# Kernel optimization log

Measured on AMD Instinct MI355X. Metric: run time of the kernel, lower is better.

Reference implementation:

```python
import jax, jax.numpy as jnp
import numpy as np

N, E = 20000, 640000
S_DIM, V_DIM, E_DIM = 128, 32 // 2, 32
EPS = 1e-8


def _vector_norm(v):
    # v: [N, V, 3] -> [N, V]
    return jnp.sqrt(jnp.clip((v * v).sum(-1), EPS))


def _gvp(s, v, W1, b1, W2, b2, Wv, Wg, bg):
    """SimpleGVP: s [N,s_in], v [N,v_in,3] -> (s_out [N,s_out], v_out [N,v_out,3]).
    Weights stored [in, out] (transpose of torch Linear)."""
    vn = _vector_norm(v)                                   # [N, v_in]
    h = jnp.concatenate([s, vn], axis=-1) @ W1 + b1        # [N, s_out]
    s_out = jax.nn.silu(h) @ W2 + b2                       # [N, s_out]
    v_proj = jnp.einsum('nvc,vw->nwc', v, Wv)              # [N, v_out, 3]
    gate = jax.nn.sigmoid(s_out @ Wg + bg)[..., None]      # [N, v_out, 1]
    return s_out, v_proj * gate


def _layer_norm(x, g, b, eps=1e-5):
    mu = x.mean(-1, keepdims=True)
    var = ((x - mu) ** 2).mean(-1, keepdims=True)
    return (x - mu) * jax.lax.rsqrt(var + eps) * g + b


def _linear_params(key, fan_in, fan_out, bias=True):
    kw, kb = jax.random.split(key)
    lim = 1.0 / np.sqrt(fan_in)
    W = jax.random.uniform(kw, (fan_in, fan_out), jnp.float32, -lim, lim)
    if bias:
        b = jax.random.uniform(kb, (fan_out,), jnp.float32, -lim, lim)
        return W, b
    return (W,)


def setup_inputs() -> dict:
    key = jax.random.key(0)
    ks = jax.random.split(key, 16)
    s = jax.random.normal(ks[0], (N, S_DIM), jnp.float32)
    v = jax.random.normal(ks[1], (N, V_DIM, 3), jnp.float32)
    edge_index = jax.random.randint(ks[2], (2, E), 0, N, jnp.int32)
    edge_s = jax.random.normal(ks[3], (E, E_DIM), jnp.float32)
    edge_v = jax.random.normal(ks[4], (E, 1, 3), jnp.float32)

    # message GVP: s_in = 2*S + E_DIM + 1 (+v_in norms), v_in = 2*V + 1
    ms_in, mv_in = 2 * S_DIM + E_DIM + 1, 2 * V_DIM + 1
    msg_W1, msg_b1 = _linear_params(ks[5], ms_in + mv_in, S_DIM)
    msg_W2, msg_b2 = _linear_params(ks[6], S_DIM, S_DIM)
    (msg_Wv,) = _linear_params(ks[7], mv_in, V_DIM, bias=False)
    msg_Wg, msg_bg = _linear_params(ks[8], S_DIM, V_DIM)

    # update GVP: s_in = 2*S, v_in = 2*V
    us_in, uv_in = 2 * S_DIM, 2 * V_DIM
    upd_W1, upd_b1 = _linear_params(ks[9], us_in + uv_in, S_DIM)
    upd_W2, upd_b2 = _linear_params(ks[10], S_DIM, S_DIM)
    (upd_Wv,) = _linear_params(ks[11], uv_in, V_DIM, bias=False)
    upd_Wg, upd_bg = _linear_params(ks[12], S_DIM, V_DIM)

    ln_g = jnp.ones((S_DIM,), jnp.float32)
    ln_b = jnp.zeros((S_DIM,), jnp.float32)

    return dict(s=s, v=v, edge_index=edge_index, edge_s=edge_s, edge_v=edge_v,
                msg_W1=msg_W1, msg_b1=msg_b1, msg_W2=msg_W2, msg_b2=msg_b2,
                msg_Wv=msg_Wv, msg_Wg=msg_Wg, msg_bg=msg_bg,
                upd_W1=upd_W1, upd_b1=upd_b1, upd_W2=upd_W2, upd_b2=upd_b2,
                upd_Wv=upd_Wv, upd_Wg=upd_Wg, upd_bg=upd_bg,
                ln_g=ln_g, ln_b=ln_b)


def reference(s, v, edge_index, edge_s, edge_v,
              msg_W1, msg_b1, msg_W2, msg_b2, msg_Wv, msg_Wg, msg_bg,
              upd_W1, upd_b1, upd_W2, upd_b2, upd_Wv, upd_Wg, upd_bg,
              ln_g, ln_b):
    src, dst = edge_index[0], edge_index[1]
    n = s.shape[0]

    # 1) per-edge message inputs (gather)
    edge_len = _vector_norm(edge_v)                                   # [E, 1]
    m_s_in = jnp.concatenate([s[src], s[dst], edge_s, edge_len], -1)  # [E, 2S+e+1]
    m_v_in = jnp.concatenate([v[src], v[dst], edge_v], 1)             # [E, 2V+1, 3]
    m_s, m_v = _gvp(m_s_in, m_v_in, msg_W1, msg_b1, msg_W2, msg_b2,
                    msg_Wv, msg_Wg, msg_bg)

    # 2) scatter-add aggregation at destination nodes
    agg_s = jax.ops.segment_sum(m_s, dst, num_segments=n)             # [N, S]
    agg_v = jax.ops.segment_sum(m_v, dst, num_segments=n)             # [N, V, 3]

    # 3) residual update
    u_s_in = jnp.concatenate([s, agg_s], -1)
    u_v_in = jnp.concatenate([v, agg_v], 1)
    ds, dv = _gvp(u_s_in, u_v_in, upd_W1, upd_b1, upd_W2, upd_b2,
                  upd_Wv, upd_Wg, upd_bg)

    s_out = _layer_norm(s + ds, ln_g, ln_b)
    v_out = v + dv
    return s_out, v_out
```

## Files before the change

kernel.cpp:

```cpp
#include <hip/hip_runtime.h>

typedef __attribute__((ext_vector_type(4))) float floatx4;
typedef __attribute__((ext_vector_type(8))) short shortx8;
typedef __attribute__((ext_vector_type(4))) short shortx4;
typedef __attribute__((ext_vector_type(4))) int intx4;
typedef __attribute__((ext_vector_type(2))) int intx2;

#define DEVI static __device__ __forceinline__

constexpr int NN = 20000;
constexpr int NE = 640000;

constexpr size_t W1ET_OFF = 0;
constexpr size_t WLEN_OFF = 8192;
constexpr size_t WCAT_OFF = 8704;
constexpr size_t W2GT_OFF = 90624;
constexpr size_t CG_OFF   = 94720;
constexpr size_t U1T_OFF  = 94784;
constexpr size_t B2U_OFF  = 168512;
constexpr size_t U2T_OFF  = 169024;
constexpr size_t UGT_OFF  = 201792;
constexpr size_t ASRC_OFF = 205888;
constexpr size_t ADST_OFF = ASRC_OFF + (size_t)NN * 128 * 2;
constexpr size_t BSRC_OFF = ADST_OFF + (size_t)NN * 128 * 2;
constexpr size_t BDST_OFF = BSRC_OFF + (size_t)NN * 64 * 2;
constexpr size_t AGG_S_OFF = BDST_OFF + (size_t)NN * 64 * 2;
constexpr size_t AGG_V_OFF = AGG_S_OFF + (size_t)NN * 128 * 2;
constexpr size_t CNT_OFF  = AGG_V_OFF + (size_t)NN * 64 * 2;
constexpr size_t OFF_OFF  = CNT_OFF + (size_t)NN * 4;
constexpr size_t PERM_OFF = OFF_OFF + (size_t)NN * 4;
constexpr size_t MEMSET_BYTES = (size_t)NN * 128 * 2 + (size_t)NN * 64 * 2 + (size_t)NN * 4;

DEVI float bf2f(short h) {
  union { unsigned u; float f; } c;
  c.u = ((unsigned)(unsigned short)h) << 16;
  return c.f;
}
DEVI short f2bf(float f) {
  union { float f; unsigned u; } c; c.f = f;
  unsigned x = c.u;
  return (short)((x + 0x7fffu + ((x >> 16) & 1u)) >> 16);
}
DEVI int pack2bf(float x, float y) {
  return (int)(unsigned short)f2bf(x) | ((int)(unsigned short)f2bf(y) << 16);
}
DEVI void atom_pk(short* addr, int val) {
  asm volatile("global_atomic_pk_add_bf16 %0, %1, off" : : "v"(addr), "v"(val) : "memory");
}
DEVI float sigm(float x) { return __builtin_amdgcn_rcpf(1.0f + __expf(-x)); }

DEVI floatx4 mfma16(shortx8 a, shortx8 b, floatx4 c) {
  return __builtin_amdgcn_mfma_f32_16x16x32_bf16(a, b, c, 0, 0, 0);
}

__global__ void gvp_prep(const float* __restrict__ mW1, const float* __restrict__ mW2,
                         const float* __restrict__ mWg, const float* __restrict__ mb2,
                         const float* __restrict__ mbg, const float* __restrict__ uW1,
                         const float* __restrict__ uW2, const float* __restrict__ uWg,
                         short* __restrict__ w1et, float* __restrict__ wlen,
                         short* __restrict__ wcat, short* __restrict__ w2gt,
                         float* __restrict__ cg, short* __restrict__ u1t,
                         float* __restrict__ b2u, short* __restrict__ u2t,
                         short* __restrict__ ugt) {
  int i = blockIdx.x * 256 + threadIdx.x;
  if (i < 4096) { int n = i >> 5, k = i & 31; w1et[i] = f2bf(mW1[(256 + k) * 128 + n]); return; }
  i -= 4096;
  if (i < 128) { wlen[i] = mW1[288 * 128 + i] + mW1[321 * 128 + i]; return; }
  i -= 128;
  if (i < 40960) {
    int n = i / 160, k = i % 160;
    float val = 0.f;
    if (n < 128) {
      if (k < 128) val = mW1[k * 128 + n];
      else if (k < 144) val = mW1[(161 + k) * 128 + n];
    } else {
      int n2 = n - 128;
      if (k < 128) val = mW1[(128 + k) * 128 + n2];
      else if (k < 144) val = mW1[(177 + k) * 128 + n2];
    }
    wcat[i] = f2bf(val);
    return;
  }
  i -= 40960;
  if (i < 2048) {
    int g = i >> 7, k = i & 127;
    float acc = 0.f;
#pragma unroll 4
    for (int c4 = 0; c4 < 32; ++c4) {
      floatx4 wr = *(const floatx4*)(mW2 + k * 128 + c4 * 4);
      acc += wr[0] * mWg[(c4 * 4 + 0) * 16 + g] + wr[1] * mWg[(c4 * 4 + 1) * 16 + g] +
             wr[2] * mWg[(c4 * 4 + 2) * 16 + g] + wr[3] * mWg[(c4 * 4 + 3) * 16 + g];
    }
    w2gt[i] = f2bf(acc);
    return;
  }
  i -= 2048;
  if (i < 16) {
    float acc = mbg[i];
    for (int c = 0; c < 128; ++c) acc += mb2[c] * mWg[c * 16 + i];
    cg[i] = acc;
    return;
  }
  i -= 16;
  if (i < 36864) {
    int n = i / 288, k = i % 288;
    if (k < 128 || k >= 256) {
      u1t[i] = f2bf(uW1[k * 128 + n]);
    } else {
      int j = k - 128;
      float acc = 0.f;
#pragma unroll 4
      for (int c4 = 0; c4 < 32; ++c4) {
        floatx4 wr = *(const floatx4*)(mW2 + j * 128 + c4 * 4);
        acc += wr[0] * uW1[(128 + c4 * 4 + 0) * 128 + n] +
               wr[1] * uW1[(128 + c4 * 4 + 1) * 128 + n] +
               wr[2] * uW1[(128 + c4 * 4 + 2) * 128 + n] +
               wr[3] * uW1[(128 + c4 * 4 + 3) * 128 + n];
      }
      u1t[i] = f2bf(acc);
    }
    return;
  }
  i -= 36864;
  if (i < 128) {
    float acc = 0.f;
    for (int c = 0; c < 128; ++c) acc += mb2[c] * uW1[(128 + c) * 128 + i];
    b2u[i] = acc;
    return;
  }
  i -= 128;
  if (i < 16384) { int n = i >> 7, k = i & 127; u2t[i] = f2bf(uW2[k * 128 + n]); return; }
  i -= 16384;
  if (i < 2048) { int g = i >> 7, k = i & 127; ugt[i] = f2bf(uWg[k * 16 + g]); return; }
}

__global__ void gvp_hist(const int* __restrict__ eidx, int* __restrict__ cnt) {
  int e = blockIdx.x * 256 + threadIdx.x;
  if (e < NE) atomicAdd(cnt + eidx[NE + e], 1);
}

__global__ void gvp_scan(const int* __restrict__ cnt, int* __restrict__ off) {
  __shared__ int part[256];
  const int t = threadIdx.x;
  const int base = t * 79;
  int sum = 0;
  for (int j = 0; j < 79; ++j) {
    int i = base + j;
    if (i < NN) sum += cnt[i];
  }
  part[t] = sum;
  __syncthreads();
  if (t == 0) {
    int run = 0;
    for (int i = 0; i < 256; ++i) { int c = part[i]; part[i] = run; run += c; }
  }
  __syncthreads();
  int run = part[t];
  for (int j = 0; j < 79; ++j) {
    int i = base + j;
    if (i < NN) { off[i] = run; run += cnt[i]; }
  }
}

__global__ void gvp_scatter(const int* __restrict__ eidx, int* __restrict__ off,
                            int* __restrict__ perm) {
  int e = blockIdx.x * 256 + threadIdx.x;
  if (e >= NE) return;
  int d = eidx[NE + e];
  int pos = atomicAdd(off + d, 1);
  perm[pos] = e;
}

__global__ __launch_bounds__(256) void gvp_nodepre(
    const float* __restrict__ s, const float* __restrict__ v,
    const short* __restrict__ wcat, const float* __restrict__ b1,
    const float* __restrict__ wv, short* __restrict__ Asrc,
    short* __restrict__ Adst, short* __restrict__ Bsrc, short* __restrict__ Bdst) {
  __shared__ __align__(16) short lx[64 * 160];
  const int tid = threadIdx.x;
  const int wid = tid >> 6;
  const int lane = tid & 63;
  const int quad = lane >> 4;
  const int l16 = lane & 15;
  const int nb0 = blockIdx.x * 64;

  intx4 z4 = {0, 0, 0, 0};
#pragma unroll
  for (int i = 0; i < 4; i++) {
    int idx = tid + i * 256;
    int r = idx >> 4, cc = (idx & 15) * 8;
    int node = nb0 + r;
    union { short sh[8]; intx4 v4; } u;
    u.v4 = z4;
    if (node < NN) {
      const float* sp = s + (size_t)node * 128 + cc;
      floatx4 f0 = *(const floatx4*)sp, f1 = *(const floatx4*)(sp + 4);
#pragma unroll
      for (int j = 0; j < 4; j++) { u.sh[j] = f2bf(f0[j]); u.sh[4 + j] = f2bf(f1[j]); }
    }
    *(intx4*)(lx + r * 160 + cc) = u.v4;
  }
  if (tid < 64) {
    int node = nb0 + tid;
    union { short sh[16]; intx4 v4[2]; } u;
#pragma unroll
    for (int j = 0; j < 16; j++) {
      float nv = 0.f;
      if (node < NN) {
        const float* vp = v + (size_t)node * 48 + j * 3;
        nv = sqrtf(fmaxf(vp[0] * vp[0] + vp[1] * vp[1] + vp[2] * vp[2], 1e-8f));
      }
      u.sh[j] = f2bf(nv);
    }
    *(intx4*)(lx + tid * 160 + 128) = u.v4[0];
    *(intx4*)(lx + tid * 160 + 136) = u.v4[1];
    *(intx4*)(lx + tid * 160 + 144) = z4;
    *(intx4*)(lx + tid * 160 + 152) = z4;
  }
  __syncthreads();

  floatx4 acc[16] = {};
#pragma unroll
  for (int kc = 0; kc < 5; kc++) {
    shortx8 a = *(const shortx8*)(lx + (wid * 16 + l16) * 160 + kc * 32 + quad * 8);
#pragma unroll
    for (int nt = 0; nt < 16; nt++) {
      shortx8 b = *(const shortx8*)(wcat + (size_t)(nt * 16 + l16) * 160 + kc * 32 + quad * 8);
      acc[nt] = mfma16(a, b, acc[nt]);
    }
  }

  float b1v[8];
#pragma unroll
  for (int nt = 0; nt < 8; nt++) b1v[nt] = b1[nt * 16 + l16];
#pragma unroll
  for (int i = 0; i < 4; i++) {
    int row = wid * 16 + quad * 4 + i;
    int node = nb0 + row;
    if (node < NN) {
      union { short sh[8]; intx4 v4; } us, ud;
#pragma unroll
      for (int nt = 0; nt < 8; nt++) {
        us.sh[nt] = f2bf(acc[nt][i] + b1v[nt]);
        ud.sh[nt] = f2bf(acc[8 + nt][i]);
      }
      *(intx4*)(Asrc + (size_t)node * 128 + l16 * 8) = us.v4;
      *(intx4*)(Adst + (size_t)node * 128 + l16 * 8) = ud.v4;
    }
  }

  {
    int node = nb0 + (tid >> 2), sub = tid & 3;
    if (node < NN) {
      float vr[48];
      const float* vp = v + (size_t)node * 48;
#pragma unroll
      for (int j = 0; j < 48; j++) vr[j] = vp[j];
      for (int w = sub * 4; w < sub * 4 + 4; w++) {
        float bs0 = 0, bs1 = 0, bs2 = 0, bd0 = 0, bd1 = 0, bd2 = 0;
#pragma unroll
        for (int j = 0; j < 16; j++) {
          float w0 = wv[j * 16 + w], w1 = wv[(16 + j) * 16 + w];
          bs0 += vr[j * 3 + 0] * w0; bs1 += vr[j * 3 + 1] * w0; bs2 += vr[j * 3 + 2] * w0;
          bd0 += vr[j * 3 + 0] * w1; bd1 += vr[j * 3 + 1] * w1; bd2 += vr[j * 3 + 2] * w1;
        }
        union { short sh[4]; intx2 v2; } ub, ud2;
        ub.sh[0] = f2bf(bs0); ub.sh[1] = f2bf(bs1); ub.sh[2] = f2bf(bs2); ub.sh[3] = 0;
        ud2.sh[0] = f2bf(bd0); ud2.sh[1] = f2bf(bd1); ud2.sh[2] = f2bf(bd2); ud2.sh[3] = 0;
        *(intx2*)(Bsrc + (size_t)node * 64 + w * 4) = ub.v2;
        *(intx2*)(Bdst + (size_t)node * 64 + w * 4) = ud2.v2;
      }
    }
  }
}

__global__ __launch_bounds__(256, 8) void gvp_edge(
    const int* __restrict__ perm, const int* __restrict__ eidx,
    const float* __restrict__ ev, const float* __restrict__ es,
    const short* __restrict__ w1et, const float* __restrict__ wlen,
    const short* __restrict__ w2gt, const short* __restrict__ Asrc,
    const short* __restrict__ Adst, const short* __restrict__ Bsrc,
    const short* __restrict__ Bdst, const float* __restrict__ cg,
    const float* __restrict__ wv, short* __restrict__ agg_s,
    short* __restrict__ agg_v) {
  __shared__ __align__(16) short lh_all[4 * 16 * 136];
  __shared__ int lpe[64];
  __shared__ int lsrc[64];
  __shared__ int ldst[64];
  __shared__ float lev4[64][4];

  const int tid = threadIdx.x;
  const int wid = tid >> 6;
  const int lane = tid & 63;
  const int quad = lane >> 4;
  const int l16 = lane & 15;
  const int e0 = blockIdx.x * 64;

  if (tid < 64) {
    int pe = perm[e0 + tid];
    lpe[tid] = pe;
    lsrc[tid] = eidx[pe];
    ldst[tid] = eidx[NE + pe];
  } else if (tid < 128) {
    int er = tid - 64;
    int pe = perm[e0 + er];
    const float* evp = ev + (size_t)pe * 3;
    float x = evp[0], y = evp[1], z = evp[2];
    lev4[er][0] = x; lev4[er][1] = y; lev4[er][2] = z;
    lev4[er][3] = sqrtf(fmaxf(x * x + y * y + z * z, 1e-8f));
  }
  __syncthreads();

  short* lh = lh_all + wid * 2176;

  const int erow = wid * 16 + l16;
  const int pe = lpe[erow];
  const float* ep = es + (size_t)pe * 32 + quad * 8;
  floatx4 ea = *(const floatx4*)ep;
  floatx4 eb = *(const floatx4*)(ep + 4);
  shortx8 afrag;
#pragma unroll
  for (int j = 0; j < 4; j++) { afrag[j] = f2bf(ea[j]); afrag[4 + j] = f2bf(eb[j]); }
  floatx4 acc[8];
#pragma unroll
  for (int nt = 0; nt < 8; nt++) {
    shortx8 b = *(const shortx8*)(w1et + (nt * 16 + l16) * 32 + quad * 8);
    floatx4 z = {0.f, 0.f, 0.f, 0.f};
    acc[nt] = mfma16(afrag, b, z);
  }

  int srcn[4], dstn[4];
  float lenr[4];
#pragma unroll
  for (int i = 0; i < 4; i++) {
    int r = wid * 16 + quad * 4 + i;
    srcn[i] = lsrc[r]; dstn[i] = ldst[r]; lenr[i] = lev4[r][3];
  }

#pragma unroll
  for (int i = 0; i < 4; i++) {
    shortx8 s8 = *(const shortx8*)(Asrc + (size_t)srcn[i] * 128 + l16 * 8);
    shortx8 d8 = *(const shortx8*)(Adst + (size_t)dstn[i] * 128 + l16 * 8);
#pragma unroll
    for (int nt = 0; nt < 8; nt++) acc[nt][i] += bf2f(s8[nt]) + bf2f(d8[nt]);
  }
#pragma unroll
  for (int nt = 0; nt < 8; nt++) {
    float wl = wlen[nt * 16 + l16];
#pragma unroll
    for (int i = 0; i < 4; i++) acc[nt][i] += lenr[i] * wl;
  }

#pragma unroll
  for (int nt = 0; nt < 8; nt++)
#pragma unroll
    for (int i = 0; i < 4; i++) {
      float h = acc[nt][i];
      lh[(quad * 4 + i) * 136 + nt * 16 + l16] = f2bf(h * sigm(h));
    }

  floatx4 acc3 = {0.f, 0.f, 0.f, 0.f};
#pragma unroll
  for (int kc = 0; kc < 4; kc++) {
    shortx8 a = *(const shortx8*)(lh + l16 * 136 + kc * 32 + quad * 8);
    shortx8 b = *(const shortx8*)(w2gt + l16 * 128 + kc * 32 + quad * 8);
    acc3 = mfma16(a, b, acc3);
  }

  float wv32v = wv[32 * 16 + l16];
  float cgv = cg[l16];
  float gv[4][3];
#pragma unroll
  for (int i = 0; i < 4; i++) {
    int r = wid * 16 + quad * 4 + i;
    shortx4 bs = *(const shortx4*)(Bsrc + (size_t)srcn[i] * 64 + l16 * 4);
    shortx4 bd = *(const shortx4*)(Bdst + (size_t)dstn[i] * 64 + l16 * 4);
    float vx = bf2f(bs[0]) + bf2f(bd[0]) + lev4[r][0] * wv32v;
    float vy = bf2f(bs[1]) + bf2f(bd[1]) + lev4[r][1] * wv32v;
    float vz = bf2f(bs[2]) + bf2f(bd[2]) + lev4[r][2] * wv32v;
    float g = sigm(acc3[i] + cgv);
    gv[i][0] = g * vx; gv[i][1] = g * vy; gv[i][2] = g * vz;
  }

  const int rbase = wid * 16;
  int r = 0;
  while (r < 16) {
    int d = ldst[rbase + r];
    int r2 = r + 1;
    while (r2 < 16 && ldst[rbase + r2] == d) ++r2;
    float s0 = 0.f, s1 = 0.f;
    for (int row = r; row < r2; ++row) {
      int pv = *(const int*)(lh + row * 136 + 2 * lane);
      s0 += bf2f((short)(pv & 0xffff));
      s1 += bf2f((short)((unsigned)pv >> 16));
    }
    atom_pk(agg_s + (size_t)d * 128 + 2 * lane, pack2bf(s0, s1));
    float vx = 0.f, vy = 0.f, vz = 0.f;
#pragma unroll
    for (int i = 0; i < 4; ++i) {
      int row = quad * 4 + i;
      if (row >= r && row < r2) { vx += gv[i][0]; vy += gv[i][1]; vz += gv[i][2]; }
    }
    vx += __shfl_xor(vx, 16); vy += __shfl_xor(vy, 16); vz += __shfl_xor(vz, 16);
    vx += __shfl_xor(vx, 32); vy += __shfl_xor(vy, 32); vz += __shfl_xor(vz, 32);
    if (quad == 0) {
      short* ap = agg_v + (size_t)d * 64 + l16 * 4;
      atom_pk(ap, pack2bf(vx, vy));
      atom_pk(ap + 2, pack2bf(vz, 0.f));
    }
    r = r2;
  }
}

__global__ __launch_bounds__(256) void gvp_node(
    const float* __restrict__ s, const float* __restrict__ v,
    const short* __restrict__ agg_s, const short* __restrict__ agg_v,
    const int* __restrict__ cnt, const float* __restrict__ b2u,
    const short* __restrict__ u1t, const short* __restrict__ u2t,
    const short* __restrict__ ugt, const float* __restrict__ b1,
    const float* __restrict__ b2, const float* __restrict__ uwv,
    const float* __restrict__ bg, const float* __restrict__ lng,
    const float* __restrict__ lnb, float* __restrict__ out_s,
    float* __restrict__ out_v) {
  __shared__ __align__(16) short lx[64 * 352];
  const int tid = threadIdx.x;
  const int wid = tid >> 6;
  const int lane = tid & 63;
  const int quad = lane >> 4;
  const int l16 = lane & 15;
  const int nb0 = blockIdx.x * 64;

  float cntf[4];
#pragma unroll
  for (int i = 0; i < 4; i++) {
    int node = nb0 + wid * 16 + quad * 4 + i;
    cntf[i] = (node < NN) ? (float)cnt[node] : 0.f;
  }

  intx4 z4 = {0, 0, 0, 0};
#pragma unroll
  for (int i = 0; i < 4; i++) {
    int idx = tid + i * 256;
    int r = idx >> 4, cc = (idx & 15) * 8;
    int node = nb0 + r;
    union { short sh[8]; intx4 v4; } u;
    u.v4 = z4;
    if (node < NN) {
      const float* sp = s + (size_t)node * 128 + cc;
      floatx4 f0 = *(const floatx4*)sp, f1 = *(const floatx4*)(sp + 4);
#pragma unroll
      for (int j = 0; j < 4; j++) { u.sh[j] = f2bf(f0[j]); u.sh[4 + j] = f2bf(f1[j]); }
    }
    *(intx4*)(lx + r * 288 + cc) = u.v4;
  }
#pragma unroll
  for (int i = 0; i < 4; i++) {
    int idx = tid + i * 256;
    int r = idx >> 4, cc = (idx & 15) * 8;
    int node = nb0 + r;
    intx4 val = z4;
    if (node < NN) val = *(const intx4*)(agg_s + (size_t)node * 128 + cc);
    *(intx4*)(lx + r * 288 + 128 + cc) = val;
  }
  {
    int r = tid >> 2, p = tid & 3;
    int node = nb0 + r;
    int w0 = (p & 1) * 8;
    if (p < 2) {
#pragma unroll
      for (int w = 0; w < 8; w++) {
        float nv = 0.f;
        if (node < NN) {
          const float* vp = v + (size_t)node * 48 + (w0 + w) * 3;
          nv = sqrtf(fmaxf(vp[0] * vp[0] + vp[1] * vp[1] + vp[2] * vp[2], 1e-8f));
        }
        lx[r * 288 + 256 + w0 + w] = f2bf(nv);
      }
    } else {
#pragma unroll
      for (int w = 0; w < 8; w++) {
        float nv = 0.f;
        if (node < NN) {
          const short* ap = agg_v + (size_t)node * 64 + (w0 + w) * 4;
          float x = bf2f(ap[0]), y = bf2f(ap[1]), zz = bf2f(ap[2]);
          nv = sqrtf(fmaxf(x * x + y * y + zz * zz, 1e-8f));
        }
        lx[r * 288 + 272 + w0 + w] = f2bf(nv);
      }
    }
  }
  __syncthreads();

  floatx4 acc[8] = {};
#pragma unroll
  for (int kc = 0; kc < 9; kc++) {
    shortx8 a = *(const shortx8*)(lx + (wid * 16 + l16) * 288 + kc * 32 + quad * 8);
#pragma unroll
    for (int nt = 0; nt < 8; nt++) {
      shortx8 b = *(const shortx8*)(u1t + (size_t)(nt * 16 + l16) * 288 + kc * 32 + quad * 8);
      acc[nt] = mfma16(a, b, acc[nt]);
    }
  }
  __syncthreads();

  short* lh = lx;
#pragma unroll
  for (int nt = 0; nt < 8; nt++)
#pragma unroll
    for (int i = 0; i < 4; i++) {
      int row = wid * 16 + quad * 4 + i;
      int col = nt * 16 + l16;
      float h = acc[nt][i] + b1[col] + cntf[i] * b2u[col];
      lh[row * 136 + col] = f2bf(h * sigm(h));
    }

  floatx4 acc2[8] = {};
#pragma unroll
  for (int kc = 0; kc < 4; kc++) {
    shortx8 a = *(const shortx8*)(lh + (wid * 16 + l16) * 136 + kc * 32 + quad * 8);
#pragma unroll
    for (int nt = 0; nt < 8; nt++) {
      shortx8 b = *(const shortx8*)(u2t + (size_t)(nt * 16 + l16) * 128 + kc * 32 + quad * 8);
      acc2[nt] = mfma16(a, b, acc2[nt]);
    }
  }

#pragma unroll
  for (int nt = 0; nt < 8; nt++)
#pragma unroll
    for (int i = 0; i < 4; i++) {
      int row = wid * 16 + quad * 4 + i;
      int col = nt * 16 + l16;
      int node = nb0 + row;
      float ds = acc2[nt][i] + b2[col];
      lh[row * 136 + col] = f2bf(ds);
      float sv = (node < NN) ? s[(size_t)node * 128 + col] : 0.f;
      acc2[nt][i] = sv + ds;
    }

#pragma unroll
  for (int i = 0; i < 4; i++) {
    float sum = 0.f, sq = 0.f;
#pragma unroll
    for (int nt = 0; nt < 8; nt++) { float t = acc2[nt][i]; sum += t; sq += t * t; }
    for (int off = 1; off < 16; off <<= 1) {
      sum += __shfl_xor(sum, off);
      sq += __shfl_xor(sq, off);
    }
    float mean = sum * (1.f / 128.f);
    float var = sq * (1.f / 128.f) - mean * mean;
    float inv = rsqrtf(fmaxf(var, 0.f) + 1e-5f);
    int node = nb0 + wid * 16 + quad * 4 + i;
    if (node < NN) {
#pragma unroll
      for (int nt = 0; nt < 8; nt++) {
        int col = nt * 16 + l16;
        float o = (acc2[nt][i] - mean) * inv * lng[col] + lnb[col];
        out_s[(size_t)node * 128 + col] = o;
      }
    }
  }

  float* lmvf = (float*)((char*)lx + 17408) + wid * 1600;
  {
    int e = lane >> 2, p = lane & 3;
    int node = nb0 + wid * 16 + e;
    if (p < 2) {
      floatx4* dp = (floatx4*)(lmvf + e * 100 + p * 24);
      if (node < NN) {
        const floatx4* sp = (const floatx4*)(v + (size_t)node * 48 + p * 24);
#pragma unroll
        for (int j = 0; j < 6; j++) dp[j] = sp[j];
      } else {
        floatx4 zf = {0.f, 0.f, 0.f, 0.f};
#pragma unroll
        for (int j = 0; j < 6; j++) dp[j] = zf;
      }
    } else {
      int wbase = (p - 2) * 8;
#pragma unroll
      for (int w = 0; w < 8; w++) {
        float x = 0.f, y = 0.f, zz = 0.f;
        if (node < NN) {
          const short* ap = agg_v + (size_t)node * 64 + (wbase + w) * 4;
          x = bf2f(ap[0]); y = bf2f(ap[1]); zz = bf2f(ap[2]);
        }
        float* dp = lmvf + e * 100 + 48 + (wbase + w) * 3;
        dp[0] = x; dp[1] = y; dp[2] = zz;
      }
    }
  }

  floatx4 acc3 = {0.f, 0.f, 0.f, 0.f};
#pragma unroll
  for (int kc = 0; kc < 4; kc++) {
    shortx8 a = *(const shortx8*)(lh + (wid * 16 + l16) * 136 + kc * 32 + quad * 8);
    shortx8 b = *(const shortx8*)(ugt + l16 * 128 + kc * 32 + quad * 8);
    acc3 = mfma16(a, b, acc3);
  }

  float vm[4][3] = {};
  for (int j = 0; j < 32; j++) {
    float wj = uwv[j * 16 + l16];
#pragma unroll
    for (int i = 0; i < 4; i++) {
      int e = quad * 4 + i;
      vm[i][0] += wj * lmvf[e * 100 + j * 3 + 0];
      vm[i][1] += wj * lmvf[e * 100 + j * 3 + 1];
      vm[i][2] += wj * lmvf[e * 100 + j * 3 + 2];
    }
  }
#pragma unroll
  for (int i = 0; i < 4; i++) {
    int node = nb0 + wid * 16 + quad * 4 + i;
    if (node < NN) {
      float g = sigm(acc3[i] + bg[l16]);
      size_t base = (size_t)node * 48 + l16 * 3;
      out_v[base + 0] = v[base + 0] + g * vm[i][0];
      out_v[base + 1] = v[base + 1] + g * vm[i][1];
      out_v[base + 2] = v[base + 2] + g * vm[i][2];
    }
  }
}

extern "C" void kernel_launch(void* const* d_in, const int* in_sizes, int n_in,
                              void* d_out, int out_size, void* d_ws, size_t ws_size,
                              hipStream_t stream) {
  const float* s = (const float*)d_in[0];
  const float* v = (const float*)d_in[1];
  const int* eidx = (const int*)d_in[2];
  const float* es = (const float*)d_in[3];
  const float* ev = (const float*)d_in[4];
  const float* mW1 = (const float*)d_in[5];
  const float* mb1 = (const float*)d_in[6];
  const float* mW2 = (const float*)d_in[7];
  const float* mb2 = (const float*)d_in[8];
  const float* mWv = (const float*)d_in[9];
  const float* mWg = (const float*)d_in[10];
  const float* mbg = (const float*)d_in[11];
  const float* uW1 = (const float*)d_in[12];
  const float* ub1 = (const float*)d_in[13];
  const float* uW2 = (const float*)d_in[14];
  const float* ub2 = (const float*)d_in[15];
  const float* uWv = (const float*)d_in[16];
  const float* uWg = (const float*)d_in[17];
  const float* ubg = (const float*)d_in[18];
  const float* lng = (const float*)d_in[19];
  const float* lnb = (const float*)d_in[20];

  char* ws = (char*)d_ws;
  short* w1et = (short*)(ws + W1ET_OFF);
  float* wlen = (float*)(ws + WLEN_OFF);
  short* wcat = (short*)(ws + WCAT_OFF);
  short* w2gt = (short*)(ws + W2GT_OFF);
  float* cg = (float*)(ws + CG_OFF);
  short* u1t = (short*)(ws + U1T_OFF);
  float* b2u = (float*)(ws + B2U_OFF);
  short* u2t = (short*)(ws + U2T_OFF);
  short* ugt = (short*)(ws + UGT_OFF);
  short* Asrc = (short*)(ws + ASRC_OFF);
  short* Adst = (short*)(ws + ADST_OFF);
  short* Bsrc = (short*)(ws + BSRC_OFF);
  short* Bdst = (short*)(ws + BDST_OFF);
  short* agg_s = (short*)(ws + AGG_S_OFF);
  short* agg_v = (short*)(ws + AGG_V_OFF);
  int* cnt = (int*)(ws + CNT_OFF);
  int* off = (int*)(ws + OFF_OFF);
  int* perm = (int*)(ws + PERM_OFF);

  hipMemsetAsync(ws + AGG_S_OFF, 0, MEMSET_BYTES, stream);
  gvp_prep<<<402, 256, 0, stream>>>(mW1, mW2, mWg, mb2, mbg, uW1, uW2, uWg,
                                    w1et, wlen, wcat, w2gt, cg, u1t, b2u, u2t, ugt);
  gvp_hist<<<NE / 256, 256, 0, stream>>>(eidx, cnt);
  gvp_scan<<<1, 256, 0, stream>>>(cnt, off);
  gvp_scatter<<<NE / 256, 256, 0, stream>>>(eidx, off, perm);
  gvp_nodepre<<<(NN + 63) / 64, 256, 0, stream>>>(s, v, wcat, mb1, mWv,
                                                  Asrc, Adst, Bsrc, Bdst);
  gvp_edge<<<NE / 64, 256, 0, stream>>>(perm, eidx, ev, es, w1et, wlen, w2gt,
                                        Asrc, Adst, Bsrc, Bdst, cg, mWv,
                                        agg_s, agg_v);
  gvp_node<<<(NN + 63) / 64, 256, 0, stream>>>(s, v, agg_s, agg_v, cnt, b2u,
                                               u1t, u2t, ugt, ub1, ub2, uWv, ubg,
                                               lng, lnb, (float*)d_out,
                                               (float*)d_out + (size_t)NN * 128);
}
```

Measured before the change: 579.3 us.

## Fuse hist/scatter into neighbor kernels, presort edge data, MFMA for node vector proj

The histogram is merged into the weight-prep launch, and the scatter step is merged into the node-precompute launch as extra blocks. The scatter also writes src/dst pairs and edge vectors plus their lengths in sorted order, so the edge kernel reads them contiguously instead of gathering through perm. In the node update kernel, the scalar fp32 vector-projection loop is replaced by bf16 MFMA against a pretransposed uWv, which reduces LDS use. This removes two launches and the random gathers, at the cost of extra workspace traffic and bf16 rounding of v in the update projection.

```diff
diff --git a/kernel.cpp b/kernel.cpp
--- a/kernel.cpp
+++ b/kernel.cpp
@@ -10,6 +10,10 @@
 
 constexpr int NN = 20000;
 constexpr int NE = 640000;
+constexpr int PREP_BLOCKS = 404;
+constexpr int HIST_BLOCKS = NE / 256;
+constexpr int SCAT_BLOCKS = NE / 256;
+constexpr int NODE_BLOCKS = (NN + 63) / 64;
 
 constexpr size_t W1ET_OFF = 0;
 constexpr size_t WLEN_OFF = 8192;
@@ -20,7 +24,8 @@
 constexpr size_t B2U_OFF  = 168512;
 constexpr size_t U2T_OFF  = 169024;
 constexpr size_t UGT_OFF  = 201792;
-constexpr size_t ASRC_OFF = 205888;
+constexpr size_t UWVT_OFF = 205888;
+constexpr size_t ASRC_OFF = 206912;
 constexpr size_t ADST_OFF = ASRC_OFF + (size_t)NN * 128 * 2;
 constexpr size_t BSRC_OFF = ADST_OFF + (size_t)NN * 128 * 2;
 constexpr size_t BDST_OFF = BSRC_OFF + (size_t)NN * 64 * 2;
@@ -29,6 +34,8 @@
 constexpr size_t CNT_OFF  = AGG_V_OFF + (size_t)NN * 64 * 2;
 constexpr size_t OFF_OFF  = CNT_OFF + (size_t)NN * 4;
 constexpr size_t PERM_OFF = OFF_OFF + (size_t)NN * 4;
+constexpr size_t SD_OFF   = PERM_OFF + (size_t)NE * 4;
+constexpr size_t LEV_OFF  = SD_OFF + (size_t)NE * 8;
 constexpr size_t MEMSET_BYTES = (size_t)NN * 128 * 2 + (size_t)NN * 64 * 2 + (size_t)NN * 4;
 
 DEVI float bf2f(short h) {
@@ -57,11 +64,18 @@
                          const float* __restrict__ mWg, const float* __restrict__ mb2,
                          const float* __restrict__ mbg, const float* __restrict__ uW1,
                          const float* __restrict__ uW2, const float* __restrict__ uWg,
+                         const float* __restrict__ uWv, const int* __restrict__ eidx,
                          short* __restrict__ w1et, float* __restrict__ wlen,
                          short* __restrict__ wcat, short* __restrict__ w2gt,
                          float* __restrict__ cg, short* __restrict__ u1t,
                          float* __restrict__ b2u, short* __restrict__ u2t,
-                         short* __restrict__ ugt) {
+                         short* __restrict__ ugt, short* __restrict__ uwvt,
+                         int* __restrict__ cnt) {
+  if (blockIdx.x >= PREP_BLOCKS) {
+    int e = (blockIdx.x - PREP_BLOCKS) * 256 + threadIdx.x;
+    if (e < NE) atomicAdd(cnt + eidx[NE + e], 1);
+    return;
+  }
   int i = blockIdx.x * 256 + threadIdx.x;
   if (i < 4096) { int n = i >> 5, k = i & 31; w1et[i] = f2bf(mW1[(256 + k) * 128 + n]); return; }
   i -= 4096;
@@ -132,11 +146,8 @@
   if (i < 16384) { int n = i >> 7, k = i & 127; u2t[i] = f2bf(uW2[k * 128 + n]); return; }
   i -= 16384;
   if (i < 2048) { int g = i >> 7, k = i & 127; ugt[i] = f2bf(uWg[k * 16 + g]); return; }
-}
-
-__global__ void gvp_hist(const int* __restrict__ eidx, int* __restrict__ cnt) {
-  int e = blockIdx.x * 256 + threadIdx.x;
-  if (e < NE) atomicAdd(cnt + eidx[NE + e], 1);
+  i -= 2048;
+  if (i < 512) { int w = i >> 5, k = i & 31; uwvt[i] = f2bf(uWv[k * 16 + w]); return; }
 }
 
 __global__ void gvp_scan(const int* __restrict__ cnt, int* __restrict__ off) {
@@ -162,27 +173,38 @@
   }
 }
 
-__global__ void gvp_scatter(const int* __restrict__ eidx, int* __restrict__ off,
-                            int* __restrict__ perm) {
-  int e = blockIdx.x * 256 + threadIdx.x;
-  if (e >= NE) return;
-  int d = eidx[NE + e];
-  int pos = atomicAdd(off + d, 1);
-  perm[pos] = e;
-}
-
 __global__ __launch_bounds__(256) void gvp_nodepre(
-    const float* __restrict__ s, const float* __restrict__ v,
-    const short* __restrict__ wcat, const float* __restrict__ b1,
-    const float* __restrict__ wv, short* __restrict__ Asrc,
-    short* __restrict__ Adst, short* __restrict__ Bsrc, short* __restrict__ Bdst) {
+    const int* __restrict__ eidx, const float* __restrict__ ev,
+    int* __restrict__ off, int* __restrict__ perm, int* __restrict__ sd,
+    float* __restrict__ lev, const float* __restrict__ s,
+    const float* __restrict__ v, const short* __restrict__ wcat,
+    const float* __restrict__ b1, const float* __restrict__ wv,
+    short* __restrict__ Asrc, short* __restrict__ Adst,
+    short* __restrict__ Bsrc, short* __restrict__ Bdst) {
   __shared__ __align__(16) short lx[64 * 160];
+  if (blockIdx.x < SCAT_BLOCKS) {
+    int e = blockIdx.x * 256 + threadIdx.x;
+    if (e < NE) {
+      int sn = eidx[e], d = eidx[NE + e];
+      int pos = atomicAdd(off + d, 1);
+      perm[pos] = e;
+      intx2 p; p[0] = sn; p[1] = d;
+      *(intx2*)(sd + (size_t)pos * 2) = p;
+      const float* evp = ev + (size_t)e * 3;
+      float x = evp[0], y = evp[1], z = evp[2];
+      floatx4 q;
+      q[0] = x; q[1] = y; q[2] = z;
+      q[3] = sqrtf(fmaxf(x * x + y * y + z * z, 1e-8f));
+      *(floatx4*)(lev + (size_t)pos * 4) = q;
+    }
+    return;
+  }
   const int tid = threadIdx.x;
   const int wid = tid >> 6;
   const int lane = tid & 63;
   const int quad = lane >> 4;
   const int l16 = lane & 15;
-  const int nb0 = blockIdx.x * 64;
+  const int nb0 = (blockIdx.x - SCAT_BLOCKS) * 64;
 
   intx4 z4 = {0, 0, 0, 0};
 #pragma unroll
@@ -275,8 +297,8 @@
 }
 
 __global__ __launch_bounds__(256, 8) void gvp_edge(
-    const int* __restrict__ perm, const int* __restrict__ eidx,
-    const float* __restrict__ ev, const float* __restrict__ es,
+    const int* __restrict__ perm, const int* __restrict__ sd,
+    const float* __restrict__ lev, const float* __restrict__ es,
     const short* __restrict__ w1et, const float* __restrict__ wlen,
     const short* __restrict__ w2gt, const short* __restrict__ Asrc,
     const short* __restrict__ Adst, const short* __restrict__ Bsrc,
@@ -297,17 +319,16 @@
   const int e0 = blockIdx.x * 64;
 
   if (tid < 64) {
-    int pe = perm[e0 + tid];
-    lpe[tid] = pe;
-    lsrc[tid] = eidx[pe];
-    ldst[tid] = eidx[NE + pe];
+    intx2 p = *(const intx2*)(sd + (size_t)(e0 + tid) * 2);
+    lsrc[tid] = p[0];
+    ldst[tid] = p[1];
   } else if (tid < 128) {
     int er = tid - 64;
-    int pe = perm[e0 + er];
-    const float* evp = ev + (size_t)pe * 3;
-    float x = evp[0], y = evp[1], z = evp[2];
-    lev4[er][0] = x; lev4[er][1] = y; lev4[er][2] = z;
-    lev4[er][3] = sqrtf(fmaxf(x * x + y * y + z * z, 1e-8f));
+    floatx4 q = *(const floatx4*)(lev + (size_t)(e0 + er) * 4);
+    lev4[er][0] = q[0]; lev4[er][1] = q[1]; lev4[er][2] = q[2]; lev4[er][3] = q[3];
+  } else if (tid < 192) {
+    int er = tid - 128;
+    lpe[er] = perm[e0 + er];
   }
   __syncthreads();
 
@@ -417,12 +438,12 @@
     const short* __restrict__ agg_s, const short* __restrict__ agg_v,
     const int* __restrict__ cnt, const float* __restrict__ b2u,
     const short* __restrict__ u1t, const short* __restrict__ u2t,
-    const short* __restrict__ ugt, const float* __restrict__ b1,
-    const float* __restrict__ b2, const float* __restrict__ uwv,
+    const short* __restrict__ ugt, const short* __restrict__ uwvt,
+    const float* __restrict__ b1, const float* __restrict__ b2,
     const float* __restrict__ bg, const float* __restrict__ lng,
     const float* __restrict__ lnb, float* __restrict__ out_s,
     float* __restrict__ out_v) {
-  __shared__ __align__(16) short lx[64 * 352];
+  __shared__ __align__(16) short lx[64 * 288];
   const int tid = threadIdx.x;
   const int wid = tid >> 6;
   const int lane = tid & 63;
@@ -504,6 +525,7 @@
   __syncthreads();
 
   short* lh = lx;
+  short* lb = lx + 8704 + wid * 1536;
 #pragma unroll
   for (int nt = 0; nt < 8; nt++)
 #pragma unroll
@@ -561,32 +583,38 @@
     }
   }
 
-  float* lmvf = (float*)((char*)lx + 17408) + wid * 1600;
   {
     int e = lane >> 2, p = lane & 3;
     int node = nb0 + wid * 16 + e;
+    short* lbe = lb + e * 32;
     if (p < 2) {
-      floatx4* dp = (floatx4*)(lmvf + e * 100 + p * 24);
+      float vr[24];
       if (node < NN) {
         const floatx4* sp = (const floatx4*)(v + (size_t)node * 48 + p * 24);
 #pragma unroll
-        for (int j = 0; j < 6; j++) dp[j] = sp[j];
+        for (int j = 0; j < 6; j++) {
+          floatx4 f = sp[j];
+          vr[j * 4 + 0] = f[0]; vr[j * 4 + 1] = f[1];
+          vr[j * 4 + 2] = f[2]; vr[j * 4 + 3] = f[3];
+        }
       } else {
-        floatx4 zf = {0.f, 0.f, 0.f, 0.f};
-#pragma unroll
-        for (int j = 0; j < 6; j++) dp[j] = zf;
-      }
+#pragma unroll
+        for (int j = 0; j < 24; j++) vr[j] = 0.f;
+      }
+#pragma unroll
+      for (int k = 0; k < 8; k++)
+#pragma unroll
+        for (int c = 0; c < 3; c++)
+          lbe[c * 512 + p * 8 + k] = f2bf(vr[k * 3 + c]);
     } else {
       int wbase = (p - 2) * 8;
 #pragma unroll
       for (int w = 0; w < 8; w++) {
-        float x = 0.f, y = 0.f, zz = 0.f;
-        if (node < NN) {
-          const short* ap = agg_v + (size_t)node * 64 + (wbase + w) * 4;
-          x = bf2f(ap[0]); y = bf2f(ap[1]); zz = bf2f(ap[2]);
-        }
-        float* dp = lmvf + e * 100 + 48 + (wbase + w) * 3;
-        dp[0] = x; dp[1] = y; dp[2] = zz;
+        shortx4 av = {0, 0, 0, 0};
+        if (node < NN) av = *(const shortx4*)(agg_v + (size_t)node * 64 + (wbase + w) * 4);
+#pragma unroll
+        for (int c = 0; c < 3; c++)
+          lbe[c * 512 + 16 + wbase + w] = av[c];
       }
     }
   }
@@ -599,17 +627,17 @@
     acc3 = mfma16(a, b, acc3);
   }
 
-  float vm[4][3] = {};
-  for (int j = 0; j < 32; j++) {
-    float wj = uwv[j * 16 + l16];
-#pragma unroll
-    for (int i = 0; i < 4; i++) {
-      int e = quad * 4 + i;
-      vm[i][0] += wj * lmvf[e * 100 + j * 3 + 0];
-      vm[i][1] += wj * lmvf[e * 100 + j * 3 + 1];
-      vm[i][2] += wj * lmvf[e * 100 + j * 3 + 2];
-    }
-  }
+  float vm[4][3];
+#pragma unroll
+  for (int c = 0; c < 3; c++) {
+    shortx8 a = *(const shortx8*)(lb + c * 512 + l16 * 32 + quad * 8);
+    shortx8 b = *(const shortx8*)(uwvt + l16 * 32 + quad * 8);
+    floatx4 z = {0.f, 0.f, 0.f, 0.f};
+    floatx4 rr = mfma16(a, b, z);
+#pragma unroll
+    for (int i = 0; i < 4; i++) vm[i][c] = rr[i];
+  }
+
 #pragma unroll
   for (int i = 0; i < 4; i++) {
     int node = nb0 + wid * 16 + quad * 4 + i;
@@ -658,6 +686,7 @@
   float* b2u = (float*)(ws + B2U_OFF);
   short* u2t = (short*)(ws + U2T_OFF);
   short* ugt = (short*)(ws + UGT_OFF);
+  short* uwvt = (short*)(ws + UWVT_OFF);
   short* Asrc = (short*)(ws + ASRC_OFF);
   short* Adst = (short*)(ws + ADST_OFF);
   short* Bsrc = (short*)(ws + BSRC_OFF);
@@ -667,20 +696,21 @@
   int* cnt = (int*)(ws + CNT_OFF);
   int* off = (int*)(ws + OFF_OFF);
   int* perm = (int*)(ws + PERM_OFF);
+  int* sd = (int*)(ws + SD_OFF);
+  float* lev = (float*)(ws + LEV_OFF);
 
   hipMemsetAsync(ws + AGG_S_OFF, 0, MEMSET_BYTES, stream);
-  gvp_prep<<<402, 256, 0, stream>>>(mW1, mW2, mWg, mb2, mbg, uW1, uW2, uWg,
-                                    w1et, wlen, wcat, w2gt, cg, u1t, b2u, u2t, ugt);
-  gvp_hist<<<NE / 256, 256, 0, stream>>>(eidx, cnt);
+  gvp_prep<<<PREP_BLOCKS + HIST_BLOCKS, 256, 0, stream>>>(
+      mW1, mW2, mWg, mb2, mbg, uW1, uW2, uWg, uWv, eidx,
+      w1et, wlen, wcat, w2gt, cg, u1t, b2u, u2t, ugt, uwvt, cnt);
   gvp_scan<<<1, 256, 0, stream>>>(cnt, off);
-  gvp_scatter<<<NE / 256, 256, 0, stream>>>(eidx, off, perm);
-  gvp_nodepre<<<(NN + 63) / 64, 256, 0, stream>>>(s, v, wcat, mb1, mWv,
-                                                  Asrc, Adst, Bsrc, Bdst);
-  gvp_edge<<<NE / 64, 256, 0, stream>>>(perm, eidx, ev, es, w1et, wlen, w2gt,
+  gvp_nodepre<<<SCAT_BLOCKS + NODE_BLOCKS, 256, 0, stream>>>(
+      eidx, ev, off, perm, sd, lev, s, v, wcat, mb1, mWv, Asrc, Adst, Bsrc, Bdst);
+  gvp_edge<<<NE / 64, 256, 0, stream>>>(perm, sd, lev, es, w1et, wlen, w2gt,
                                         Asrc, Adst, Bsrc, Bdst, cg, mWv,
                                         agg_s, agg_v);
-  gvp_node<<<(NN + 63) / 64, 256, 0, stream>>>(s, v, agg_s, agg_v, cnt, b2u,
-                                               u1t, u2t, ugt, ub1, ub2, uWv, ubg,
-                                               lng, lnb, (float*)d_out,
-                                               (float*)d_out + (size_t)NN * 128);
-}
+  gvp_node<<<NODE_BLOCKS, 256, 0, stream>>>(s, v, agg_s, agg_v, cnt, b2u,
+                                            u1t, u2t, ugt, uwvt, ub1, ub2, ubg,
+                                            lng, lnb, (float*)d_out,
+                                            (float*)d_out + (size_t)NN * 128);
+}
```

After: 563.4 us. -2.7%, faster.
